# Kernel tuning notes

Measured on AMD Instinct MI355X. Metric: run time of the kernel, lower is better.

Reference implementation:

```python
import jax, jax.numpy as jnp
import numpy as np

S1, S2, B, H, E, IN, OUT, NL = 8, 32, 256, 1024, 512, 2, 2, 4


def setup_inputs() -> dict:
    key = jax.random.key(0)
    ks = jax.random.split(key, 20)
    s_h = 1.0 / np.sqrt(H)
    inp = {
        'input': jax.random.normal(ks[0], (B, IN), jnp.float32),
        'h0': jax.random.normal(ks[1], (NL, B, H), jnp.float32) * 0.5,
        'c0': jax.random.normal(ks[2], (NL, B, H), jnp.float32) * 0.5,
        'all_outputs': jax.random.normal(ks[3], (S1, S2, B, H), jnp.float32),
        'W_emb': jax.random.normal(ks[4], (E, IN), jnp.float32) / np.sqrt(IN),
        'b_emb': jax.random.normal(ks[5], (E,), jnp.float32) * 0.01,
        'W_attn': jax.random.normal(ks[6], (1, 2 * H), jnp.float32) / np.sqrt(2 * H),
        'b_attn': jax.random.normal(ks[7], (1,), jnp.float32) * 0.01,
        'Wih0': jax.random.normal(ks[8], (4 * H, E + H), jnp.float32) / np.sqrt(E + H),
        'Whh0': jax.random.normal(ks[9], (4 * H, H), jnp.float32) * s_h,
        'bih0': jax.random.normal(ks[10], (4 * H,), jnp.float32) * 0.01,
        'bhh0': jax.random.normal(ks[11], (4 * H,), jnp.float32) * 0.01,
        'Wih_r': jax.random.normal(ks[12], (NL - 1, 4 * H, H), jnp.float32) * s_h,
        'Whh_r': jax.random.normal(ks[13], (NL - 1, 4 * H, H), jnp.float32) * s_h,
        'bih_r': jax.random.normal(ks[14], (NL - 1, 4 * H), jnp.float32) * 0.01,
        'bhh_r': jax.random.normal(ks[15], (NL - 1, 4 * H), jnp.float32) * 0.01,
        'W_out': jax.random.normal(ks[16], (OUT, H), jnp.float32) * s_h,
        'b_out': jax.random.normal(ks[17], (OUT,), jnp.float32) * 0.01,
    }
    return inp


def _lstm_cell(x, h, c, Wih, Whh, bih, bhh):
    g = x @ Wih.T + h @ Whh.T + bih + bhh  # [B, 4H], torch gate order i,f,g,o
    i, f, gg, o = jnp.split(g, 4, axis=1)
    c2 = jax.nn.sigmoid(f) * c + jax.nn.sigmoid(i) * jnp.tanh(gg)
    h2 = jax.nn.sigmoid(o) * jnp.tanh(c2)
    return h2, c2


def reference(input, h0, c0, all_outputs, W_emb, b_emb, W_attn, b_attn,
              Wih0, Whh0, bih0, bhh0, Wih_r, Whh_r, bih_r, bhh_r, W_out, b_out):
    s1, s2, b, h_dim = all_outputs.shape
    # embedding (dropout = identity in eval mode)
    embedded = jax.nn.relu(input @ W_emb.T + b_emb)  # [B, E]
    h_top = h0[0]  # [B, H]
    # attn(cat(h_top, y)) decomposed: h part is shared across all (j, i)
    w_h = W_attn[0, :h_dim]
    w_y = W_attn[0, h_dim:]
    scores = (jnp.einsum('jibh,h->jib', all_outputs, w_y)
              + (h_top @ w_h)[None, None, :] + b_attn[0])  # [S1, S2, B]
    # torch cats per-(j,i) [B,1] columns j-major -> [B, S1*S2]
    normalized = jax.nn.softmax(scores.reshape(s1 * s2, b).T, axis=1)  # [B, S1*S2]
    temp = normalized.reshape(b, s1, s2)
    # NOTE: original writes into an expand()-ed zero buffer, so every j-slice
    # aliases the same memory; after the loop all slices equal the last j's bmm
    # result and sum(0) multiplies it by S1. We replicate that exactly.
    applied_last = jnp.einsum('bi,ibh->bh', temp[:, -1, :], all_outputs[-1])  # [B, H]
    final_attn = s1 * applied_last
    x = jnp.concatenate([final_attn, embedded], axis=1)  # [B, H+E]
    hs, cs = [], []
    h, c = _lstm_cell(x, h0[0], c0[0], Wih0, Whh0, bih0, bhh0)
    hs.append(h); cs.append(c)
    for l in range(Wih_r.shape[0]):  # inter-layer dropout = identity in eval
        h, c = _lstm_cell(h, h0[l + 1], c0[l + 1], Wih_r[l], Whh_r[l], bih_r[l], bhh_r[l])
        hs.append(h); cs.append(c)
    h_new = jnp.stack(hs)
    c_new = jnp.stack(cs)
    final_output = h @ W_out.T + b_out  # [B, OUT]
    return final_output, h_new, c_new, normalized
```

## Files before the change

### kernel.cpp

```cpp
#include <hip/hip_runtime.h>
#include <hip/hip_bf16.h>

typedef __bf16 bf16x8 __attribute__((ext_vector_type(8)));
typedef float  f32x4  __attribute__((ext_vector_type(4)));

#define O_FINAL 0
#define O_H     512
#define O_C     1049088
#define O_NORM  2097664

__device__ __forceinline__ bf16x8 cvt8(float4 a, float4 b) {
  bf16x8 r;
  r[0] = (__bf16)a.x; r[1] = (__bf16)a.y; r[2] = (__bf16)a.z; r[3] = (__bf16)a.w;
  r[4] = (__bf16)b.x; r[5] = (__bf16)b.y; r[6] = (__bf16)b.z; r[7] = (__bf16)b.w;
  return r;
}

template<int K>
__device__ __forceinline__ void tile_gemm_bf(const __bf16* __restrict__ A,
                                             const float* __restrict__ W,
                                             int r0, int j0, char* lds,
                                             f32x4 acc[2]) {
  constexpr int NK = K / 64;
  constexpr int D = 4;
  const int t = threadIdx.x, lane = t & 63, wave = t >> 6;
  const int rf = wave & 3, gg = wave >> 2;
  const int tr = t >> 3, chunk = t & 7;
  const float*  wsrc = W + (size_t)((tr >> 4) * 1024 + j0 + (tr & 15)) * K + chunk * 8;
  const __bf16* asrc = A + (size_t)(r0 + tr) * K + chunk * 8;
  const int sw_off = (chunk ^ (tr & 7)) << 4;
  const int woff = 8192 + tr * 128 + sw_off;
  const int aoff = tr * 128 + sw_off;
  const int a_tr  = rf * 16 + (lane & 15);
  const int w_tr0 = gg * 32 + (lane & 15);
  const int w_tr1 = w_tr0 + 16;
  const int ksel  = lane >> 4;

  float4 wp[D][2]; bf16x8 ap[D];
#pragma unroll
  for (int d = 0; d < D; ++d) {
    wp[d][0] = *(const float4*)(wsrc + d * 64);
    wp[d][1] = *(const float4*)(wsrc + d * 64 + 4);
    ap[d]    = *(const bf16x8*)(asrc + d * 64);
  }
#pragma unroll
  for (int s = 0; s < NK; ++s) {
    const int sl = s % D;
    char* buf = lds + (s & 1) * 16384;
    *(bf16x8*)(buf + aoff) = ap[sl];
    *(bf16x8*)(buf + woff) = cvt8(wp[sl][0], wp[sl][1]);
    if (s + D < NK) {
      wp[sl][0] = *(const float4*)(wsrc + (s + D) * 64);
      wp[sl][1] = *(const float4*)(wsrc + (s + D) * 64 + 4);
      ap[sl]    = *(const bf16x8*)(asrc + (s + D) * 64);
    }
    __syncthreads();
#pragma unroll
    for (int s2 = 0; s2 < 2; ++s2) {
      const int chk = s2 * 4 + ksel;
      bf16x8 af  = *(const bf16x8*)(buf + a_tr * 128 + ((chk ^ (a_tr & 7)) << 4));
      bf16x8 wf0 = *(const bf16x8*)(buf + 8192 + w_tr0 * 128 + ((chk ^ (w_tr0 & 7)) << 4));
      bf16x8 wf1 = *(const bf16x8*)(buf + 8192 + w_tr1 * 128 + ((chk ^ (w_tr1 & 7)) << 4));
      acc[0] = __builtin_amdgcn_mfma_f32_16x16x32_bf16(af, wf0, acc[0], 0, 0, 0);
      acc[1] = __builtin_amdgcn_mfma_f32_16x16x32_bf16(af, wf1, acc[1], 0, 0, 0);
    }
  }
}

template<int K>
__device__ __forceinline__ void tile_gemm_ff(const float* __restrict__ A,
                                             const float* __restrict__ W,
                                             int r0, int j0, char* lds,
                                             f32x4 acc[2]) {
  constexpr int NK = K / 64;
  constexpr int D = 4;
  const int t = threadIdx.x, lane = t & 63, wave = t >> 6;
  const int rf = wave & 3, gg = wave >> 2;
  const int tr = t >> 3, chunk = t & 7;
  const float* wsrc = W + (size_t)((tr >> 4) * 1024 + j0 + (tr & 15)) * K + chunk * 8;
  const float* asrc = A + (size_t)(r0 + tr) * K + chunk * 8;
  const int sw_off = (chunk ^ (tr & 7)) << 4;
  const int woff = 8192 + tr * 128 + sw_off;
  const int aoff = tr * 128 + sw_off;
  const int a_tr  = rf * 16 + (lane & 15);
  const int w_tr0 = gg * 32 + (lane & 15);
  const int w_tr1 = w_tr0 + 16;
  const int ksel  = lane >> 4;

  float4 wp[D][2], ap[D][2];
#pragma unroll
  for (int d = 0; d < D; ++d) {
    wp[d][0] = *(const float4*)(wsrc + d * 64);
    wp[d][1] = *(const float4*)(wsrc + d * 64 + 4);
    ap[d][0] = *(const float4*)(asrc + d * 64);
    ap[d][1] = *(const float4*)(asrc + d * 64 + 4);
  }
#pragma unroll
  for (int s = 0; s < NK; ++s) {
    const int sl = s % D;
    char* buf = lds + (s & 1) * 16384;
    *(bf16x8*)(buf + aoff) = cvt8(ap[sl][0], ap[sl][1]);
    *(bf16x8*)(buf + woff) = cvt8(wp[sl][0], wp[sl][1]);
    if (s + D < NK) {
      wp[sl][0] = *(const float4*)(wsrc + (s + D) * 64);
      wp[sl][1] = *(const float4*)(wsrc + (s + D) * 64 + 4);
      ap[sl][0] = *(const float4*)(asrc + (s + D) * 64);
      ap[sl][1] = *(const float4*)(asrc + (s + D) * 64 + 4);
    }
    __syncthreads();
#pragma unroll
    for (int s2 = 0; s2 < 2; ++s2) {
      const int chk = s2 * 4 + ksel;
      bf16x8 af  = *(const bf16x8*)(buf + a_tr * 128 + ((chk ^ (a_tr & 7)) << 4));
      bf16x8 wf0 = *(const bf16x8*)(buf + 8192 + w_tr0 * 128 + ((chk ^ (w_tr0 & 7)) << 4));
      bf16x8 wf1 = *(const bf16x8*)(buf + 8192 + w_tr1 * 128 + ((chk ^ (w_tr1 & 7)) << 4));
      acc[0] = __builtin_amdgcn_mfma_f32_16x16x32_bf16(af, wf0, acc[0], 0, 0, 0);
      acc[1] = __builtin_amdgcn_mfma_f32_16x16x32_bf16(af, wf1, acc[1], 0, 0, 0);
    }
  }
}

__global__ __launch_bounds__(512) void k_scores(const float* __restrict__ AO,
                                                const float* __restrict__ Wattn,
                                                float* __restrict__ sc) {
  const int lane = threadIdx.x & 63, wave = threadIdx.x >> 6;
  const float* wy = Wattn + 1024;
  float4 wv[4];
#pragma unroll
  for (int q = 0; q < 4; ++q) wv[q] = *(const float4*)(wy + lane * 4 + 256 * q);
  const int row0 = (blockIdx.x * 8 + wave) * 4;
  float a4[4];
#pragma unroll
  for (int rr = 0; rr < 4; ++rr) {
    const float4* rp = (const float4*)(AO + (size_t)(row0 + rr) * 1024);
    float a = 0.f;
#pragma unroll
    for (int q = 0; q < 4; ++q) {
      float4 v = rp[lane + 64 * q];
      a += v.x * wv[q].x + v.y * wv[q].y + v.z * wv[q].z + v.w * wv[q].w;
    }
    a4[rr] = a;
  }
#pragma unroll
  for (int rr = 0; rr < 4; ++rr) {
    float a = a4[rr];
#pragma unroll
    for (int off = 32; off; off >>= 1) a += __shfl_xor(a, off, 64);
    if (lane == 0) {
      int row = row0 + rr;
      sc[(row & 255) * 256 + (row >> 8)] = a;
    }
  }
}

__global__ __launch_bounds__(256) void k_smx(const float* __restrict__ sc,
                                             const float* __restrict__ AO,
                                             const float* __restrict__ inp,
                                             const float* __restrict__ Wemb,
                                             const float* __restrict__ bemb,
                                             float* __restrict__ norm_out,
                                             __bf16* __restrict__ x) {
  __shared__ float red[4];
  __shared__ float wsm[32];
  const int b = blockIdx.x, t = threadIdx.x, lane = t & 63, wave = t >> 6;
  float s = sc[b * 256 + t];
  float m = s;
#pragma unroll
  for (int off = 32; off; off >>= 1) m = fmaxf(m, __shfl_xor(m, off, 64));
  if (lane == 0) red[wave] = m;
  __syncthreads();
  m = fmaxf(fmaxf(red[0], red[1]), fmaxf(red[2], red[3]));
  float e = __expf(s - m);
  float sum = e;
#pragma unroll
  for (int off = 32; off; off >>= 1) sum += __shfl_xor(sum, off, 64);
  __syncthreads();
  if (lane == 0) red[wave] = sum;
  __syncthreads();
  sum = red[0] + red[1] + red[2] + red[3];
  float nv = e / sum;
  norm_out[b * 256 + t] = nv;
  if (t >= 224) wsm[t - 224] = nv;
  __syncthreads();
  float acc[4] = {0.f, 0.f, 0.f, 0.f};
  const float* base = AO + ((size_t)224 * 256 + b) * 1024;
#pragma unroll 4
  for (int i = 0; i < 32; ++i) {
    float w = wsm[i];
    const float* rp = base + (size_t)i * 262144;
#pragma unroll
    for (int q = 0; q < 4; ++q) acc[q] += w * rp[t + 256 * q];
  }
#pragma unroll
  for (int q = 0; q < 4; ++q) x[(size_t)b * 1536 + t + 256 * q] = (__bf16)(8.0f * acc[q]);
  float i0 = inp[b * 2], i1 = inp[b * 2 + 1];
#pragma unroll
  for (int r = 0; r < 2; ++r) {
    int jj = t + 256 * r;
    float e2 = i0 * Wemb[jj * 2] + i1 * Wemb[jj * 2 + 1] + bemb[jj];
    x[(size_t)b * 1536 + 1024 + jj] = (__bf16)fmaxf(e2, 0.f);
  }
}

template<int KA>
__global__ __launch_bounds__(512) void k_layer(const __bf16* __restrict__ A,
                                               const float* __restrict__ Wih,
                                               const float* __restrict__ h0l,
                                               const float* __restrict__ Whh,
                                               const float* __restrict__ bi,
                                               const float* __restrict__ bh,
                                               const float* __restrict__ c0l,
                                               float* __restrict__ h_out,
                                               float* __restrict__ c_out,
                                               __bf16* __restrict__ hb) {
  __shared__ char smem[40960];
  float* exch = (float*)(smem + 32768);
  const int t = threadIdx.x, lane = t & 63, wave = t >> 6;
  const int rf = wave & 3, gg = wave >> 2;
  const int cb = blockIdx.x & 63, rb = blockIdx.x >> 6;
  const int j0 = cb * 16, r0 = rb * 64;
  f32x4 acc[2] = {};
  tile_gemm_bf<KA>(A, Wih, r0, j0, smem, acc);
  tile_gemm_ff<1024>(h0l, Whh, r0, j0, smem, acc);
  const int col = j0 + (lane & 15);
  const int rbase = r0 + rf * 16 + ((lane >> 4) << 2);
  const int eidx = ((lane >> 4) << 2) * 16 + (lane & 15);
#pragma unroll
  for (int gi = 0; gi < 2; ++gi) {
    const int cg = (gg * 2 + gi) * 1024 + col;
    const float bsum = bi[cg] + bh[cg];
    acc[gi][0] += bsum; acc[gi][1] += bsum; acc[gi][2] += bsum; acc[gi][3] += bsum;
  }
  if (gg == 1) {
#pragma unroll
    for (int gi = 0; gi < 2; ++gi)
#pragma unroll
      for (int q = 0; q < 4; ++q)
        exch[(rf * 2 + gi) * 256 + eidx + q * 16] = acc[gi][q];
  }
  __syncthreads();
  if (gg == 0) {
#pragma unroll
    for (int q = 0; q < 4; ++q) {
      const int row = rbase + q;
      float gv = exch[(rf * 2 + 0) * 256 + eidx + q * 16];
      float ov = exch[(rf * 2 + 1) * 256 + eidx + q * 16];
      float si = 1.f / (1.f + __expf(-acc[0][q]));
      float sf = 1.f / (1.f + __expf(-acc[1][q]));
      float so = 1.f / (1.f + __expf(-ov));
      float c2 = sf * c0l[(size_t)row * 1024 + col] + si * tanhf(gv);
      float h2 = so * tanhf(c2);
      h_out[(size_t)row * 1024 + col] = h2;
      c_out[(size_t)row * 1024 + col] = c2;
      hb[(size_t)row * 1024 + col] = (__bf16)h2;
    }
  }
}

__global__ __launch_bounds__(256) void k_final(const float* __restrict__ h3,
                                               const float* __restrict__ Wout,
                                               const float* __restrict__ bout,
                                               float* __restrict__ out) {
  const int lane = threadIdx.x & 63, wave = threadIdx.x >> 6;
  const int b = blockIdx.x * 4 + wave;
  const float4* hp = (const float4*)(h3 + (size_t)b * 1024);
  const float4* w0 = (const float4*)Wout;
  const float4* w1 = (const float4*)(Wout + 1024);
  float a0 = 0.f, a1 = 0.f;
#pragma unroll
  for (int q = 0; q < 4; ++q) {
    float4 hv = hp[lane + 64 * q];
    float4 v0 = w0[lane + 64 * q];
    float4 v1 = w1[lane + 64 * q];
    a0 += hv.x * v0.x + hv.y * v0.y + hv.z * v0.z + hv.w * v0.w;
    a1 += hv.x * v1.x + hv.y * v1.y + hv.z * v1.z + hv.w * v1.w;
  }
#pragma unroll
  for (int off = 32; off; off >>= 1) {
    a0 += __shfl_xor(a0, off, 64);
    a1 += __shfl_xor(a1, off, 64);
  }
  if (lane == 0) {
    out[b * 2]     = a0 + bout[0];
    out[b * 2 + 1] = a1 + bout[1];
  }
}

extern "C" void kernel_launch(void* const* d_in, const int* in_sizes, int n_in,
                              void* d_out, int out_size, void* d_ws, size_t ws_size,
                              hipStream_t stream) {
  const float* inp    = (const float*)d_in[0];
  const float* h0     = (const float*)d_in[1];
  const float* c0     = (const float*)d_in[2];
  const float* AO     = (const float*)d_in[3];
  const float* Wemb   = (const float*)d_in[4];
  const float* bemb   = (const float*)d_in[5];
  const float* Wattn  = (const float*)d_in[6];
  const float* Wih0   = (const float*)d_in[8];
  const float* Whh0   = (const float*)d_in[9];
  const float* bih0   = (const float*)d_in[10];
  const float* bhh0   = (const float*)d_in[11];
  const float* Wih_r  = (const float*)d_in[12];
  const float* Whh_r  = (const float*)d_in[13];
  const float* bih_r  = (const float*)d_in[14];
  const float* bhh_r  = (const float*)d_in[15];
  const float* Wout   = (const float*)d_in[16];
  const float* bout   = (const float*)d_in[17];

  float* out = (float*)d_out;
  char* ws = (char*)d_ws;

  float*  sc = (float*)ws;
  __bf16* xb = (__bf16*)(ws + 262144);
  __bf16* hb = (__bf16*)(ws + 1048576);

  k_scores<<<2048, 512, 0, stream>>>(AO, Wattn, sc);
  k_smx<<<256, 256, 0, stream>>>(sc, AO, inp, Wemb, bemb, out + O_NORM, xb);

  k_layer<1536><<<256, 512, 0, stream>>>(xb, Wih0, h0, Whh0, bih0, bhh0, c0,
                                         out + O_H, out + O_C, hb);
  for (int l = 1; l < 4; ++l)
    k_layer<1024><<<256, 512, 0, stream>>>(hb + (size_t)(l - 1) * 262144,
                                           Wih_r + (size_t)(l - 1) * 4194304,
                                           h0 + (size_t)l * 262144,
                                           Whh_r + (size_t)(l - 1) * 4194304,
                                           bih_r + (size_t)(l - 1) * 4096,
                                           bhh_r + (size_t)(l - 1) * 4096,
                                           c0 + (size_t)l * 262144,
                                           out + O_H + (size_t)l * 262144,
                                           out + O_C + (size_t)l * 262144,
                                           hb + (size_t)l * 262144);

  k_final<<<64, 256, 0, stream>>>(out + O_H + 3 * 262144, Wout, bout, out + O_FINAL);
}
```

Baseline: 153.2 us.

## Precompute all layers' recurrent h0·Whh gates alongside attention scores, halve layer tiles

The recurrent term h0[l]·Whh[l]^T plus biases does not depend on earlier layers, so all four layers' versions are now computed in a merged front kernel alongside the attention-score pass and stored as a float gate buffer. Each serial layer kernel then only does the input GEMM, adds the stored gates, and applies the LSTM cell, taking the Whh work off the critical dependency chain. Layer tiles shrink to 32 rows with one gate per wave pair and twice as many blocks, giving more parallelism. In exchange, a 16MB intermediate gate buffer is written and read back, and the total weight traffic stays the same.

```diff
diff --git a/kernel.cpp b/kernel.cpp
--- a/kernel.cpp
+++ b/kernel.cpp
@@ -14,57 +14,6 @@
   r[0] = (__bf16)a.x; r[1] = (__bf16)a.y; r[2] = (__bf16)a.z; r[3] = (__bf16)a.w;
   r[4] = (__bf16)b.x; r[5] = (__bf16)b.y; r[6] = (__bf16)b.z; r[7] = (__bf16)b.w;
   return r;
-}
-
-template<int K>
-__device__ __forceinline__ void tile_gemm_bf(const __bf16* __restrict__ A,
-                                             const float* __restrict__ W,
-                                             int r0, int j0, char* lds,
-                                             f32x4 acc[2]) {
-  constexpr int NK = K / 64;
-  constexpr int D = 4;
-  const int t = threadIdx.x, lane = t & 63, wave = t >> 6;
-  const int rf = wave & 3, gg = wave >> 2;
-  const int tr = t >> 3, chunk = t & 7;
-  const float*  wsrc = W + (size_t)((tr >> 4) * 1024 + j0 + (tr & 15)) * K + chunk * 8;
-  const __bf16* asrc = A + (size_t)(r0 + tr) * K + chunk * 8;
-  const int sw_off = (chunk ^ (tr & 7)) << 4;
-  const int woff = 8192 + tr * 128 + sw_off;
-  const int aoff = tr * 128 + sw_off;
-  const int a_tr  = rf * 16 + (lane & 15);
-  const int w_tr0 = gg * 32 + (lane & 15);
-  const int w_tr1 = w_tr0 + 16;
-  const int ksel  = lane >> 4;
-
-  float4 wp[D][2]; bf16x8 ap[D];
-#pragma unroll
-  for (int d = 0; d < D; ++d) {
-    wp[d][0] = *(const float4*)(wsrc + d * 64);
-    wp[d][1] = *(const float4*)(wsrc + d * 64 + 4);
-    ap[d]    = *(const bf16x8*)(asrc + d * 64);
-  }
-#pragma unroll
-  for (int s = 0; s < NK; ++s) {
-    const int sl = s % D;
-    char* buf = lds + (s & 1) * 16384;
-    *(bf16x8*)(buf + aoff) = ap[sl];
-    *(bf16x8*)(buf + woff) = cvt8(wp[sl][0], wp[sl][1]);
-    if (s + D < NK) {
-      wp[sl][0] = *(const float4*)(wsrc + (s + D) * 64);
-      wp[sl][1] = *(const float4*)(wsrc + (s + D) * 64 + 4);
-      ap[sl]    = *(const bf16x8*)(asrc + (s + D) * 64);
-    }
-    __syncthreads();
-#pragma unroll
-    for (int s2 = 0; s2 < 2; ++s2) {
-      const int chk = s2 * 4 + ksel;
-      bf16x8 af  = *(const bf16x8*)(buf + a_tr * 128 + ((chk ^ (a_tr & 7)) << 4));
-      bf16x8 wf0 = *(const bf16x8*)(buf + 8192 + w_tr0 * 128 + ((chk ^ (w_tr0 & 7)) << 4));
-      bf16x8 wf1 = *(const bf16x8*)(buf + 8192 + w_tr1 * 128 + ((chk ^ (w_tr1 & 7)) << 4));
-      acc[0] = __builtin_amdgcn_mfma_f32_16x16x32_bf16(af, wf0, acc[0], 0, 0, 0);
-      acc[1] = __builtin_amdgcn_mfma_f32_16x16x32_bf16(af, wf1, acc[1], 0, 0, 0);
-    }
-  }
 }
 
 template<int K>
@@ -120,36 +69,66 @@
   }
 }
 
-__global__ __launch_bounds__(512) void k_scores(const float* __restrict__ AO,
-                                                const float* __restrict__ Wattn,
-                                                float* __restrict__ sc) {
-  const int lane = threadIdx.x & 63, wave = threadIdx.x >> 6;
-  const float* wy = Wattn + 1024;
-  float4 wv[4];
-#pragma unroll
-  for (int q = 0; q < 4; ++q) wv[q] = *(const float4*)(wy + lane * 4 + 256 * q);
-  const int row0 = (blockIdx.x * 8 + wave) * 4;
-  float a4[4];
-#pragma unroll
-  for (int rr = 0; rr < 4; ++rr) {
-    const float4* rp = (const float4*)(AO + (size_t)(row0 + rr) * 1024);
-    float a = 0.f;
-#pragma unroll
-    for (int q = 0; q < 4; ++q) {
-      float4 v = rp[lane + 64 * q];
-      a += v.x * wv[q].x + v.y * wv[q].y + v.z * wv[q].z + v.w * wv[q].w;
-    }
-    a4[rr] = a;
-  }
-#pragma unroll
-  for (int rr = 0; rr < 4; ++rr) {
-    float a = a4[rr];
-#pragma unroll
-    for (int off = 32; off; off >>= 1) a += __shfl_xor(a, off, 64);
-    if (lane == 0) {
-      int row = row0 + rr;
-      sc[(row & 255) * 256 + (row >> 8)] = a;
-    }
+__global__ __launch_bounds__(512) void k_front(
+    const float* __restrict__ AO, const float* __restrict__ Wattn,
+    float* __restrict__ sc,
+    const float* __restrict__ h0,
+    const float* __restrict__ Whh0, const float* __restrict__ Whh_r,
+    const float* __restrict__ bih0, const float* __restrict__ bhh0,
+    const float* __restrict__ bih_r, const float* __restrict__ bhh_r,
+    float* __restrict__ Gh) {
+  const int t = threadIdx.x, lane = t & 63, wave = t >> 6;
+  if (blockIdx.x < 2048) {
+    const float* wy = Wattn + 1024;
+    float4 wv[4];
+#pragma unroll
+    for (int q = 0; q < 4; ++q) wv[q] = *(const float4*)(wy + lane * 4 + 256 * q);
+    const int row0 = (blockIdx.x * 8 + wave) * 4;
+    float a4[4];
+#pragma unroll
+    for (int rr = 0; rr < 4; ++rr) {
+      const float4* rp = (const float4*)(AO + (size_t)(row0 + rr) * 1024);
+      float a = 0.f;
+#pragma unroll
+      for (int q = 0; q < 4; ++q) {
+        float4 v = rp[lane + 64 * q];
+        a += v.x * wv[q].x + v.y * wv[q].y + v.z * wv[q].z + v.w * wv[q].w;
+      }
+      a4[rr] = a;
+    }
+#pragma unroll
+    for (int rr = 0; rr < 4; ++rr) {
+      float a = a4[rr];
+#pragma unroll
+      for (int off = 32; off; off >>= 1) a += __shfl_xor(a, off, 64);
+      if (lane == 0) {
+        int row = row0 + rr;
+        sc[(row & 255) * 256 + (row >> 8)] = a;
+      }
+    }
+    return;
+  }
+  __shared__ char smem[32768];
+  const int j = blockIdx.x - 2048;
+  const int l = j >> 8, inner = j & 255;
+  const int cb = inner & 63, rb = inner >> 6;
+  const int j0 = cb * 16, r0 = rb * 64;
+  const float* A  = h0 + (size_t)l * 262144;
+  const float* W  = (l == 0) ? Whh0 : (Whh_r + (size_t)(l - 1) * 4194304);
+  const float* bi = (l == 0) ? bih0 : (bih_r + (size_t)(l - 1) * 4096);
+  const float* bh = (l == 0) ? bhh0 : (bhh_r + (size_t)(l - 1) * 4096);
+  f32x4 acc[2] = {};
+  tile_gemm_ff<1024>(A, W, r0, j0, smem, acc);
+  float* Go = Gh + (size_t)l * 1048576;
+  const int rf = wave & 3, gg = wave >> 2;
+  const int col = j0 + (lane & 15);
+  const int rbase = r0 + rf * 16 + ((lane >> 4) << 2);
+#pragma unroll
+  for (int gi = 0; gi < 2; ++gi) {
+    const int cg = (gg * 2 + gi) * 1024 + col;
+#pragma unroll
+    for (int q = 0; q < 4; ++q)
+      Go[(size_t)(rbase + q) * 4096 + cg] = acc[gi][q] + bi[cg] + bh[cg];
   }
 }
 
@@ -205,49 +184,80 @@
 template<int KA>
 __global__ __launch_bounds__(512) void k_layer(const __bf16* __restrict__ A,
                                                const float* __restrict__ Wih,
-                                               const float* __restrict__ h0l,
-                                               const float* __restrict__ Whh,
-                                               const float* __restrict__ bi,
-                                               const float* __restrict__ bh,
+                                               const float* __restrict__ Gh,
                                                const float* __restrict__ c0l,
                                                float* __restrict__ h_out,
                                                float* __restrict__ c_out,
                                                __bf16* __restrict__ hb) {
-  __shared__ char smem[40960];
-  float* exch = (float*)(smem + 32768);
+  constexpr int NK = KA / 64;
+  constexpr int D = 4;
+  __shared__ char smem[30720];
+  float* exch = (float*)(smem + 24576);
   const int t = threadIdx.x, lane = t & 63, wave = t >> 6;
-  const int rf = wave & 3, gg = wave >> 2;
+  const int rf = wave & 1, g = wave >> 1;
   const int cb = blockIdx.x & 63, rb = blockIdx.x >> 6;
-  const int j0 = cb * 16, r0 = rb * 64;
-  f32x4 acc[2] = {};
-  tile_gemm_bf<KA>(A, Wih, r0, j0, smem, acc);
-  tile_gemm_ff<1024>(h0l, Whh, r0, j0, smem, acc);
+  const int j0 = cb * 16, r0 = rb * 32;
+  const int tr = t >> 3, chunk = t & 7;
+  const float* wsrc = Wih + (size_t)((tr >> 4) * 1024 + j0 + (tr & 15)) * KA + chunk * 8;
+  const int woff = 4096 + tr * 128 + ((chunk ^ (tr & 7)) << 4);
+  const __bf16* asrc = A + (size_t)(r0 + (t >> 3)) * KA + chunk * 8;
+  const int aoff = (t >> 3) * 128 + ((chunk ^ ((t >> 3) & 7)) << 4);
+  const bool do_a = (t < 256);
+  const int a_tr = rf * 16 + (lane & 15);
+  const int w_tr = g * 16 + (lane & 15);
+  const int ksel = lane >> 4;
+
+  float4 wp[D][2]; bf16x8 ap[D];
+#pragma unroll
+  for (int d = 0; d < D; ++d) {
+    wp[d][0] = *(const float4*)(wsrc + d * 64);
+    wp[d][1] = *(const float4*)(wsrc + d * 64 + 4);
+    if (do_a) ap[d] = *(const bf16x8*)(asrc + d * 64);
+  }
+  f32x4 acc = {0.f, 0.f, 0.f, 0.f};
+#pragma unroll
+  for (int s = 0; s < NK; ++s) {
+    const int sl = s % D;
+    char* buf = smem + (s & 1) * 12288;
+    if (do_a) *(bf16x8*)(buf + aoff) = ap[sl];
+    *(bf16x8*)(buf + woff) = cvt8(wp[sl][0], wp[sl][1]);
+    if (s + D < NK) {
+      wp[sl][0] = *(const float4*)(wsrc + (s + D) * 64);
+      wp[sl][1] = *(const float4*)(wsrc + (s + D) * 64 + 4);
+      if (do_a) ap[sl] = *(const bf16x8*)(asrc + (s + D) * 64);
+    }
+    __syncthreads();
+#pragma unroll
+    for (int s2 = 0; s2 < 2; ++s2) {
+      const int chk = s2 * 4 + ksel;
+      bf16x8 af = *(const bf16x8*)(buf + a_tr * 128 + ((chk ^ (a_tr & 7)) << 4));
+      bf16x8 wf = *(const bf16x8*)(buf + 4096 + w_tr * 128 + ((chk ^ (w_tr & 7)) << 4));
+      acc = __builtin_amdgcn_mfma_f32_16x16x32_bf16(af, wf, acc, 0, 0, 0);
+    }
+  }
   const int col = j0 + (lane & 15);
   const int rbase = r0 + rf * 16 + ((lane >> 4) << 2);
   const int eidx = ((lane >> 4) << 2) * 16 + (lane & 15);
 #pragma unroll
-  for (int gi = 0; gi < 2; ++gi) {
-    const int cg = (gg * 2 + gi) * 1024 + col;
-    const float bsum = bi[cg] + bh[cg];
-    acc[gi][0] += bsum; acc[gi][1] += bsum; acc[gi][2] += bsum; acc[gi][3] += bsum;
-  }
-  if (gg == 1) {
-#pragma unroll
-    for (int gi = 0; gi < 2; ++gi)
-#pragma unroll
-      for (int q = 0; q < 4; ++q)
-        exch[(rf * 2 + gi) * 256 + eidx + q * 16] = acc[gi][q];
-  }
-  __syncthreads();
-  if (gg == 0) {
+  for (int q = 0; q < 4; ++q)
+    acc[q] += Gh[(size_t)(rbase + q) * 4096 + g * 1024 + col];
+  __syncthreads();
+  if (g > 0) {
+#pragma unroll
+    for (int q = 0; q < 4; ++q)
+      exch[((g - 1) * 2 + rf) * 256 + eidx + q * 16] = acc[q];
+  }
+  __syncthreads();
+  if (g == 0) {
 #pragma unroll
     for (int q = 0; q < 4; ++q) {
       const int row = rbase + q;
-      float gv = exch[(rf * 2 + 0) * 256 + eidx + q * 16];
-      float ov = exch[(rf * 2 + 1) * 256 + eidx + q * 16];
-      float si = 1.f / (1.f + __expf(-acc[0][q]));
-      float sf = 1.f / (1.f + __expf(-acc[1][q]));
-      float so = 1.f / (1.f + __expf(-ov));
+      float gf = exch[(0 * 2 + rf) * 256 + eidx + q * 16];
+      float gv = exch[(1 * 2 + rf) * 256 + eidx + q * 16];
+      float go = exch[(2 * 2 + rf) * 256 + eidx + q * 16];
+      float si = 1.f / (1.f + __expf(-acc[q]));
+      float sf = 1.f / (1.f + __expf(-gf));
+      float so = 1.f / (1.f + __expf(-go));
       float c2 = sf * c0l[(size_t)row * 1024 + col] + si * tanhf(gv);
       float h2 = so * tanhf(c2);
       h_out[(size_t)row * 1024 + col] = h2;
@@ -311,21 +321,20 @@
   char* ws = (char*)d_ws;
 
   float*  sc = (float*)ws;
-  __bf16* xb = (__bf16*)(ws + 262144);
-  __bf16* hb = (__bf16*)(ws + 1048576);
-
-  k_scores<<<2048, 512, 0, stream>>>(AO, Wattn, sc);
+  float*  Gh = (float*)(ws + 262144);
+  __bf16* xb = (__bf16*)(ws + 17039360);
+  __bf16* hb = (__bf16*)(ws + 17825792);
+
+  k_front<<<3072, 512, 0, stream>>>(AO, Wattn, sc, h0, Whh0, Whh_r,
+                                    bih0, bhh0, bih_r, bhh_r, Gh);
   k_smx<<<256, 256, 0, stream>>>(sc, AO, inp, Wemb, bemb, out + O_NORM, xb);
 
-  k_layer<1536><<<256, 512, 0, stream>>>(xb, Wih0, h0, Whh0, bih0, bhh0, c0,
+  k_layer<1536><<<512, 512, 0, stream>>>(xb, Wih0, Gh, c0,
                                          out + O_H, out + O_C, hb);
   for (int l = 1; l < 4; ++l)
-    k_layer<1024><<<256, 512, 0, stream>>>(hb + (size_t)(l - 1) * 262144,
+    k_layer<1024><<<512, 512, 0, stream>>>(hb + (size_t)(l - 1) * 262144,
                                            Wih_r + (size_t)(l - 1) * 4194304,
-                                           h0 + (size_t)l * 262144,
-                                           Whh_r + (size_t)(l - 1) * 4194304,
-                                           bih_r + (size_t)(l - 1) * 4096,
-                                           bhh_r + (size_t)(l - 1) * 4096,
+                                           Gh + (size_t)l * 1048576,
                                            c0 + (size_t)l * 262144,
                                            out + O_H + (size_t)l * 262144,
                                            out + O_C + (size_t)l * 262144,
```

Measured after the change: 164.6 us. 1.07x slower.

## Precompute all layers' recurrent h0·Whh gates in one wide kernel alongside softmax

Applied to the files above, without the earlier changes.

The h0·Whh products for all four LSTM layers do not depend on the layer chain, so they are hoisted into a new k_mid kernel. It launches 1024 GEMM tiles plus 256 softmax/attention blocks together and writes the gate pre-activations (with biases) to a workspace buffer. Each per-layer kernel then only computes the input GEMM and adds the precomputed gates, which shortens the serial critical path and fills the GPU with more parallel blocks. The cost is an extra 16 MB fp32 gate buffer that is written and read back, and k_scores also moves to 256-thread blocks.

```diff
diff --git a/kernel.cpp b/kernel.cpp
--- a/kernel.cpp
+++ b/kernel.cpp
@@ -14,57 +14,6 @@
   r[0] = (__bf16)a.x; r[1] = (__bf16)a.y; r[2] = (__bf16)a.z; r[3] = (__bf16)a.w;
   r[4] = (__bf16)b.x; r[5] = (__bf16)b.y; r[6] = (__bf16)b.z; r[7] = (__bf16)b.w;
   return r;
-}
-
-template<int K>
-__device__ __forceinline__ void tile_gemm_bf(const __bf16* __restrict__ A,
-                                             const float* __restrict__ W,
-                                             int r0, int j0, char* lds,
-                                             f32x4 acc[2]) {
-  constexpr int NK = K / 64;
-  constexpr int D = 4;
-  const int t = threadIdx.x, lane = t & 63, wave = t >> 6;
-  const int rf = wave & 3, gg = wave >> 2;
-  const int tr = t >> 3, chunk = t & 7;
-  const float*  wsrc = W + (size_t)((tr >> 4) * 1024 + j0 + (tr & 15)) * K + chunk * 8;
-  const __bf16* asrc = A + (size_t)(r0 + tr) * K + chunk * 8;
-  const int sw_off = (chunk ^ (tr & 7)) << 4;
-  const int woff = 8192 + tr * 128 + sw_off;
-  const int aoff = tr * 128 + sw_off;
-  const int a_tr  = rf * 16 + (lane & 15);
-  const int w_tr0 = gg * 32 + (lane & 15);
-  const int w_tr1 = w_tr0 + 16;
-  const int ksel  = lane >> 4;
-
-  float4 wp[D][2]; bf16x8 ap[D];
-#pragma unroll
-  for (int d = 0; d < D; ++d) {
-    wp[d][0] = *(const float4*)(wsrc + d * 64);
-    wp[d][1] = *(const float4*)(wsrc + d * 64 + 4);
-    ap[d]    = *(const bf16x8*)(asrc + d * 64);
-  }
-#pragma unroll
-  for (int s = 0; s < NK; ++s) {
-    const int sl = s % D;
-    char* buf = lds + (s & 1) * 16384;
-    *(bf16x8*)(buf + aoff) = ap[sl];
-    *(bf16x8*)(buf + woff) = cvt8(wp[sl][0], wp[sl][1]);
-    if (s + D < NK) {
-      wp[sl][0] = *(const float4*)(wsrc + (s + D) * 64);
-      wp[sl][1] = *(const float4*)(wsrc + (s + D) * 64 + 4);
-      ap[sl]    = *(const bf16x8*)(asrc + (s + D) * 64);
-    }
-    __syncthreads();
-#pragma unroll
-    for (int s2 = 0; s2 < 2; ++s2) {
-      const int chk = s2 * 4 + ksel;
-      bf16x8 af  = *(const bf16x8*)(buf + a_tr * 128 + ((chk ^ (a_tr & 7)) << 4));
-      bf16x8 wf0 = *(const bf16x8*)(buf + 8192 + w_tr0 * 128 + ((chk ^ (w_tr0 & 7)) << 4));
-      bf16x8 wf1 = *(const bf16x8*)(buf + 8192 + w_tr1 * 128 + ((chk ^ (w_tr1 & 7)) << 4));
-      acc[0] = __builtin_amdgcn_mfma_f32_16x16x32_bf16(af, wf0, acc[0], 0, 0, 0);
-      acc[1] = __builtin_amdgcn_mfma_f32_16x16x32_bf16(af, wf1, acc[1], 0, 0, 0);
-    }
-  }
 }
 
 template<int K>
@@ -120,7 +69,7 @@
   }
 }
 
-__global__ __launch_bounds__(512) void k_scores(const float* __restrict__ AO,
+__global__ __launch_bounds__(256) void k_scores(const float* __restrict__ AO,
                                                 const float* __restrict__ Wattn,
                                                 float* __restrict__ sc) {
   const int lane = threadIdx.x & 63, wave = threadIdx.x >> 6;
@@ -128,7 +77,7 @@
   float4 wv[4];
 #pragma unroll
   for (int q = 0; q < 4; ++q) wv[q] = *(const float4*)(wy + lane * 4 + 256 * q);
-  const int row0 = (blockIdx.x * 8 + wave) * 4;
+  const int row0 = (blockIdx.x * 4 + wave) * 4;
   float a4[4];
 #pragma unroll
   for (int rr = 0; rr < 4; ++rr) {
@@ -153,62 +102,89 @@
   }
 }
 
-__global__ __launch_bounds__(256) void k_smx(const float* __restrict__ sc,
-                                             const float* __restrict__ AO,
-                                             const float* __restrict__ inp,
-                                             const float* __restrict__ Wemb,
-                                             const float* __restrict__ bemb,
-                                             float* __restrict__ norm_out,
-                                             __bf16* __restrict__ x) {
-  __shared__ float red[4];
-  __shared__ float wsm[32];
-  const int b = blockIdx.x, t = threadIdx.x, lane = t & 63, wave = t >> 6;
-  float s = sc[b * 256 + t];
+__global__ __launch_bounds__(512) void k_mid(
+    const float* __restrict__ sc,   const float* __restrict__ AO,
+    const float* __restrict__ inp,  const float* __restrict__ Wemb,
+    const float* __restrict__ bemb,
+    const float* __restrict__ h0,
+    const float* __restrict__ Whh0, const float* __restrict__ Whh_r,
+    const float* __restrict__ bih0, const float* __restrict__ bhh0,
+    const float* __restrict__ bih_r, const float* __restrict__ bhh_r,
+    float* __restrict__ Gh,
+    float* __restrict__ norm_out,   __bf16* __restrict__ xb) {
+  __shared__ char smem[32768];
+  const int t = threadIdx.x, lane = t & 63, wave = t >> 6;
+  if (blockIdx.x < 1024) {
+    const int j = blockIdx.x;
+    const int l = j >> 8, inner = j & 255;
+    const int cb = inner & 63, rb = inner >> 6;
+    const int j0 = cb * 16, r0 = rb * 64;
+    const float* A  = h0 + (size_t)l * 262144;
+    const float* W  = (l == 0) ? Whh0 : (Whh_r + (size_t)(l - 1) * 4194304);
+    const float* bi = (l == 0) ? bih0 : (bih_r + (size_t)(l - 1) * 4096);
+    const float* bh = (l == 0) ? bhh0 : (bhh_r + (size_t)(l - 1) * 4096);
+    f32x4 acc[2] = {};
+    tile_gemm_ff<1024>(A, W, r0, j0, smem, acc);
+    float* Go = Gh + (size_t)l * 1048576;
+    const int rf = wave & 3, gg = wave >> 2;
+    const int col = j0 + (lane & 15);
+    const int rbase = r0 + rf * 16 + ((lane >> 4) << 2);
+#pragma unroll
+    for (int gi = 0; gi < 2; ++gi) {
+      const int cg = (gg * 2 + gi) * 1024 + col;
+#pragma unroll
+      for (int q = 0; q < 4; ++q)
+        Go[(size_t)(rbase + q) * 4096 + cg] = acc[gi][q] + bi[cg] + bh[cg];
+    }
+    return;
+  }
+  float* red  = (float*)smem;
+  float* nv_l = (float*)(smem + 64);
+  const int b = blockIdx.x - 1024;
+  float s = (t < 256) ? sc[b * 256 + t] : -3.4e38f;
   float m = s;
 #pragma unroll
   for (int off = 32; off; off >>= 1) m = fmaxf(m, __shfl_xor(m, off, 64));
   if (lane == 0) red[wave] = m;
   __syncthreads();
-  m = fmaxf(fmaxf(red[0], red[1]), fmaxf(red[2], red[3]));
-  float e = __expf(s - m);
+  m = red[0];
+#pragma unroll
+  for (int w2 = 1; w2 < 8; ++w2) m = fmaxf(m, red[w2]);
+  float e = (t < 256) ? __expf(s - m) : 0.f;
   float sum = e;
 #pragma unroll
   for (int off = 32; off; off >>= 1) sum += __shfl_xor(sum, off, 64);
   __syncthreads();
   if (lane == 0) red[wave] = sum;
   __syncthreads();
-  sum = red[0] + red[1] + red[2] + red[3];
+  sum = red[0];
+#pragma unroll
+  for (int w2 = 1; w2 < 8; ++w2) sum += red[w2];
   float nv = e / sum;
-  norm_out[b * 256 + t] = nv;
-  if (t >= 224) wsm[t - 224] = nv;
+  if (t < 256) {
+    norm_out[b * 256 + t] = nv;
+    if (t >= 224) nv_l[t - 224] = nv;
+  }
   __syncthreads();
-  float acc[4] = {0.f, 0.f, 0.f, 0.f};
+  float a0 = 0.f, a1 = 0.f;
   const float* base = AO + ((size_t)224 * 256 + b) * 1024;
 #pragma unroll 4
   for (int i = 0; i < 32; ++i) {
-    float w = wsm[i];
+    float w = nv_l[i];
     const float* rp = base + (size_t)i * 262144;
-#pragma unroll
-    for (int q = 0; q < 4; ++q) acc[q] += w * rp[t + 256 * q];
-  }
-#pragma unroll
-  for (int q = 0; q < 4; ++q) x[(size_t)b * 1536 + t + 256 * q] = (__bf16)(8.0f * acc[q]);
-  float i0 = inp[b * 2], i1 = inp[b * 2 + 1];
-#pragma unroll
-  for (int r = 0; r < 2; ++r) {
-    int jj = t + 256 * r;
-    float e2 = i0 * Wemb[jj * 2] + i1 * Wemb[jj * 2 + 1] + bemb[jj];
-    x[(size_t)b * 1536 + 1024 + jj] = (__bf16)fmaxf(e2, 0.f);
-  }
+    a0 += w * rp[t];
+    a1 += w * rp[t + 512];
+  }
+  xb[(size_t)b * 1536 + t]       = (__bf16)(8.0f * a0);
+  xb[(size_t)b * 1536 + t + 512] = (__bf16)(8.0f * a1);
+  float e2 = inp[b * 2] * Wemb[t * 2] + inp[b * 2 + 1] * Wemb[t * 2 + 1] + bemb[t];
+  xb[(size_t)b * 1536 + 1024 + t] = (__bf16)fmaxf(e2, 0.f);
 }
 
 template<int KA>
 __global__ __launch_bounds__(512) void k_layer(const __bf16* __restrict__ A,
                                                const float* __restrict__ Wih,
-                                               const float* __restrict__ h0l,
-                                               const float* __restrict__ Whh,
-                                               const float* __restrict__ bi,
-                                               const float* __restrict__ bh,
+                                               const float* __restrict__ Gh,
                                                const float* __restrict__ c0l,
                                                float* __restrict__ h_out,
                                                float* __restrict__ c_out,
@@ -219,40 +195,82 @@
   const int rf = wave & 3, gg = wave >> 2;
   const int cb = blockIdx.x & 63, rb = blockIdx.x >> 6;
   const int j0 = cb * 16, r0 = rb * 64;
-  f32x4 acc[2] = {};
-  tile_gemm_bf<KA>(A, Wih, r0, j0, smem, acc);
-  tile_gemm_ff<1024>(h0l, Whh, r0, j0, smem, acc);
-  const int col = j0 + (lane & 15);
-  const int rbase = r0 + rf * 16 + ((lane >> 4) << 2);
-  const int eidx = ((lane >> 4) << 2) * 16 + (lane & 15);
-#pragma unroll
-  for (int gi = 0; gi < 2; ++gi) {
-    const int cg = (gg * 2 + gi) * 1024 + col;
-    const float bsum = bi[cg] + bh[cg];
-    acc[gi][0] += bsum; acc[gi][1] += bsum; acc[gi][2] += bsum; acc[gi][3] += bsum;
-  }
-  if (gg == 1) {
-#pragma unroll
-    for (int gi = 0; gi < 2; ++gi)
-#pragma unroll
-      for (int q = 0; q < 4; ++q)
-        exch[(rf * 2 + gi) * 256 + eidx + q * 16] = acc[gi][q];
-  }
-  __syncthreads();
-  if (gg == 0) {
-#pragma unroll
-    for (int q = 0; q < 4; ++q) {
-      const int row = rbase + q;
-      float gv = exch[(rf * 2 + 0) * 256 + eidx + q * 16];
-      float ov = exch[(rf * 2 + 1) * 256 + eidx + q * 16];
-      float si = 1.f / (1.f + __expf(-acc[0][q]));
-      float sf = 1.f / (1.f + __expf(-acc[1][q]));
-      float so = 1.f / (1.f + __expf(-ov));
-      float c2 = sf * c0l[(size_t)row * 1024 + col] + si * tanhf(gv);
-      float h2 = so * tanhf(c2);
-      h_out[(size_t)row * 1024 + col] = h2;
-      c_out[(size_t)row * 1024 + col] = c2;
-      hb[(size_t)row * 1024 + col] = (__bf16)h2;
+  {
+    constexpr int NK = KA / 64;
+    constexpr int D = 4;
+    const int tr = t >> 3, chunk = t & 7;
+    const float*  wsrc = Wih + (size_t)((tr >> 4) * 1024 + j0 + (tr & 15)) * KA + chunk * 8;
+    const __bf16* asrc = A + (size_t)(r0 + tr) * KA + chunk * 8;
+    const int sw_off = (chunk ^ (tr & 7)) << 4;
+    const int woff = 8192 + tr * 128 + sw_off;
+    const int aoff = tr * 128 + sw_off;
+    const int a_tr  = rf * 16 + (lane & 15);
+    const int w_tr0 = gg * 32 + (lane & 15);
+    const int w_tr1 = w_tr0 + 16;
+    const int ksel  = lane >> 4;
+    f32x4 acc[2] = {};
+    float4 wp[D][2]; bf16x8 ap[D];
+#pragma unroll
+    for (int d = 0; d < D; ++d) {
+      wp[d][0] = *(const float4*)(wsrc + d * 64);
+      wp[d][1] = *(const float4*)(wsrc + d * 64 + 4);
+      ap[d]    = *(const bf16x8*)(asrc + d * 64);
+    }
+#pragma unroll
+    for (int s = 0; s < NK; ++s) {
+      const int sl = s % D;
+      char* buf = smem + (s & 1) * 16384;
+      *(bf16x8*)(buf + aoff) = ap[sl];
+      *(bf16x8*)(buf + woff) = cvt8(wp[sl][0], wp[sl][1]);
+      if (s + D < NK) {
+        wp[sl][0] = *(const float4*)(wsrc + (s + D) * 64);
+        wp[sl][1] = *(const float4*)(wsrc + (s + D) * 64 + 4);
+        ap[sl]    = *(const bf16x8*)(asrc + (s + D) * 64);
+      }
+      __syncthreads();
+#pragma unroll
+      for (int s2 = 0; s2 < 2; ++s2) {
+        const int chk = s2 * 4 + ksel;
+        bf16x8 af  = *(const bf16x8*)(buf + a_tr * 128 + ((chk ^ (a_tr & 7)) << 4));
+        bf16x8 wf0 = *(const bf16x8*)(buf + 8192 + w_tr0 * 128 + ((chk ^ (w_tr0 & 7)) << 4));
+        bf16x8 wf1 = *(const bf16x8*)(buf + 8192 + w_tr1 * 128 + ((chk ^ (w_tr1 & 7)) << 4));
+        acc[0] = __builtin_amdgcn_mfma_f32_16x16x32_bf16(af, wf0, acc[0], 0, 0, 0);
+        acc[1] = __builtin_amdgcn_mfma_f32_16x16x32_bf16(af, wf1, acc[1], 0, 0, 0);
+      }
+    }
+    const int col = j0 + (lane & 15);
+    const int rbase = r0 + rf * 16 + ((lane >> 4) << 2);
+    const int eidx = ((lane >> 4) << 2) * 16 + (lane & 15);
+#pragma unroll
+    for (int gi = 0; gi < 2; ++gi) {
+      const float* gp = Gh + (size_t)rbase * 4096 + (gg * 2 + gi) * 1024 + col;
+#pragma unroll
+      for (int q = 0; q < 4; ++q) acc[gi][q] += gp[(size_t)q * 4096];
+    }
+    __syncthreads();
+    if (gg == 1) {
+#pragma unroll
+      for (int gi = 0; gi < 2; ++gi)
+#pragma unroll
+        for (int q = 0; q < 4; ++q)
+          exch[(rf * 2 + gi) * 256 + eidx + q * 16] = acc[gi][q];
+    }
+    __syncthreads();
+    if (gg == 0) {
+#pragma unroll
+      for (int q = 0; q < 4; ++q) {
+        const int row = rbase + q;
+        float gv = exch[(rf * 2 + 0) * 256 + eidx + q * 16];
+        float ov = exch[(rf * 2 + 1) * 256 + eidx + q * 16];
+        float si = 1.f / (1.f + __expf(-acc[0][q]));
+        float sf = 1.f / (1.f + __expf(-acc[1][q]));
+        float so = 1.f / (1.f + __expf(-ov));
+        float c2 = sf * c0l[(size_t)row * 1024 + col] + si * tanhf(gv);
+        float h2 = so * tanhf(c2);
+        h_out[(size_t)row * 1024 + col] = h2;
+        c_out[(size_t)row * 1024 + col] = c2;
+        hb[(size_t)row * 1024 + col] = (__bf16)h2;
+      }
     }
   }
 }
@@ -311,21 +329,21 @@
   char* ws = (char*)d_ws;
 
   float*  sc = (float*)ws;
-  __bf16* xb = (__bf16*)(ws + 262144);
-  __bf16* hb = (__bf16*)(ws + 1048576);
-
-  k_scores<<<2048, 512, 0, stream>>>(AO, Wattn, sc);
-  k_smx<<<256, 256, 0, stream>>>(sc, AO, inp, Wemb, bemb, out + O_NORM, xb);
-
-  k_layer<1536><<<256, 512, 0, stream>>>(xb, Wih0, h0, Whh0, bih0, bhh0, c0,
+  float*  Gh = (float*)(ws + 262144);
+  __bf16* xb = (__bf16*)(ws + 17039360);
+  __bf16* hb = (__bf16*)(ws + 17825792);
+
+  k_scores<<<4096, 256, 0, stream>>>(AO, Wattn, sc);
+  k_mid<<<1280, 512, 0, stream>>>(sc, AO, inp, Wemb, bemb, h0, Whh0, Whh_r,
+                                  bih0, bhh0, bih_r, bhh_r, Gh,
+                                  out + O_NORM, xb);
+
+  k_layer<1536><<<256, 512, 0, stream>>>(xb, Wih0, Gh, c0,
                                          out + O_H, out + O_C, hb);
   for (int l = 1; l < 4; ++l)
     k_layer<1024><<<256, 512, 0, stream>>>(hb + (size_t)(l - 1) * 262144,
                                            Wih_r + (size_t)(l - 1) * 4194304,
-                                           h0 + (size_t)l * 262144,
-                                           Whh_r + (size_t)(l - 1) * 4194304,
-                                           bih_r + (size_t)(l - 1) * 4096,
-                                           bhh_r + (size_t)(l - 1) * 4096,
+                                           Gh + (size_t)l * 1048576,
                                            c0 + (size_t)l * 262144,
                                            out + O_H + (size_t)l * 262144,
                                            out + O_C + (size_t)l * 262144,
```

After: 152.3 us (median of 2 runs). About the same (-0.6%).
